# Optimization experiments

Measured on AMD Instinct MI355X. Metric: run time of the kernel, lower is better.

## Reference

```python
import jax, jax.numpy as jnp
import numpy as np

N, D, H, F, E = 2048, 1024, 16, 4096, 16
DH = D // H
CAP_F = 1.25
EPS = 1e-5

def _ln(x, w, b):
    mu = jnp.mean(x, -1, keepdims=True)
    var = jnp.mean((x - mu) ** 2, -1, keepdims=True)
    return (x - mu) * jax.lax.rsqrt(var + EPS) * w + b

def setup_inputs() -> dict:
    key = jax.random.key(0)
    ks = jax.random.split(key, 16)
    s = 0.02
    w = lambda k, shape: jax.random.normal(k, shape, jnp.float32) * s
    z = lambda *shape: jnp.zeros(shape, jnp.float32)
    return {
        'x': jax.random.normal(ks[0], (N, D), jnp.float32),
        'wk': w(ks[1], (D, D)), 'bk': z(D),
        'wq': w(ks[2], (D, D)), 'bq': z(D),
        'wv': w(ks[3], (D, D)), 'bv': z(D),
        'ipw': w(ks[4], (3 * D, D)), 'ipb': z(3 * D),
        'opw': w(ks[5], (D, D)), 'opb': z(D),
        'ln1_w': jnp.ones((D,), jnp.float32), 'ln1_b': z(D),
        'ln2_w': jnp.ones((D,), jnp.float32), 'ln2_b': z(D),
        'router_w': w(ks[6], (E, D)), 'router_b': z(E),
        'w1': w(ks[7], (E, F, D)), 'b1': z(E, F),
        'w2': w(ks[8], (E, D, F)), 'b2': z(E, D),
        'causal_mask': jnp.triu(jnp.ones((N, N), bool), k=1),  # True = masked
    }

def reference(x, wk, bk, wq, bq, wv, bv, ipw, ipb, opw, opb,
              ln1_w, ln1_b, ln2_w, ln2_b, router_w, router_b,
              w1, b1, w2, b2, causal_mask):
    n = x.shape[0]
    # --- MHA sublayer (pre-norm). NOTE: original calls multihead_attn(K, Q, V),
    # so query = W_key(h), key = W_query(h), value = W_value(h).
    h = _ln(x, ln1_w, ln1_b)
    q_in = h @ wk.T + bk
    k_in = h @ wq.T + bq
    v_in = h @ wv.T + bv
    q = (q_in @ ipw[:D].T + ipb[:D]).reshape(n, H, DH)
    k = (k_in @ ipw[D:2 * D].T + ipb[D:2 * D]).reshape(n, H, DH)
    v = (v_in @ ipw[2 * D:].T + ipb[2 * D:]).reshape(n, H, DH)
    scores = jnp.einsum('nhd,mhd->hnm', q, k) / jnp.sqrt(jnp.float32(DH))
    scores = jnp.where(causal_mask[None], -jnp.inf, scores)
    attn = jax.nn.softmax(scores, axis=-1)
    ctx = jnp.einsum('hnm,mhd->nhd', attn, v).reshape(n, D)
    x = x + ctx @ opw.T + opb
    # --- MoE FFN sublayer (pre-norm), top-1 routing with capacity drop.
    h = _ln(x, ln2_w, ln2_b)
    probs = jax.nn.softmax(h @ router_w.T + router_b, axis=-1)  # [N, E]
    p_max = jnp.max(probs, axis=-1)
    routes = jnp.argmax(probs, axis=-1)
    cap = int(CAP_F * n / E)
    onehot = jax.nn.one_hot(routes, E, dtype=jnp.int32)
    pos = jnp.cumsum(onehot, axis=0)[jnp.arange(n), routes] - 1  # position within expert
    keep = pos < cap
    slot = jnp.where(keep, routes * cap + pos, E * cap)  # dropped -> trash row
    buf = jnp.zeros((E * cap + 1, D), h.dtype).at[slot].set(h)
    xe = buf[:E * cap].reshape(E, cap, D)
    h1 = jax.nn.relu(jnp.einsum('ecd,efd->ecf', xe, w1) + b1[:, None, :])
    ye = jnp.einsum('ecf,edf->ecd', h1, w2) + b2[:, None, :]
    ybuf = jnp.concatenate([ye.reshape(E * cap, D), jnp.zeros((1, D), h.dtype)], 0)
    y = jnp.where(keep[:, None], ybuf[slot], h)  # dropped tokens pass through
    return x + y * p_max[:, None]  # is_scale_prob=True
```

## Files before the change

kernel.cpp:

```cpp
#include <hip/hip_runtime.h>
#include <hip/hip_bf16.h>


typedef unsigned int u32;
typedef unsigned short u16;
typedef __attribute__((ext_vector_type(8))) u16 u16x8;
typedef __attribute__((ext_vector_type(4))) float f32x4;
typedef __attribute__((ext_vector_type(8))) __bf16 bf16x8;

#define N_TOK 2048
#define DMODEL 1024
#define FEXP 4096
#define NEXP 16
#define CAP 160

__device__ __forceinline__ float b2f(u16 u) {
  u32 x = ((u32)u) << 16;
  return __builtin_bit_cast(float, x);
}
__device__ __forceinline__ u16 f2b(float f) {
  u32 i = __builtin_bit_cast(u32, f);
  u32 r = (i + 0x7fffu + ((i >> 16) & 1u)) >> 16;
  return (u16)r;
}

__device__ __forceinline__ f32x4 mfma16(u16x8 a, u16x8 b, f32x4 c) {
  return __builtin_amdgcn_mfma_f32_16x16x32_bf16(
      __builtin_bit_cast(bf16x8, a), __builtin_bit_cast(bf16x8, b), c, 0, 0, 0);
}

__device__ __forceinline__ void gll16(const void* g, void* lds) {
  __builtin_amdgcn_global_load_lds(
      (const __attribute__((address_space(1))) u32*)(unsigned long long)(uintptr_t)g,
      (__attribute__((address_space(3))) u32*)(u32)(uintptr_t)lds, 16, 0, 0);
}

__global__ __launch_bounds__(256) void split_kernel(const float *s, u16 *hi, u16 *lo, int n4) {
  const int i = blockIdx.x * 256 + threadIdx.x;
  if (i >= n4) return;
  const float4 v = ((const float4 *)s)[i];
  const u16 h0 = f2b(v.x), h1 = f2b(v.y), h2 = f2b(v.z), h3 = f2b(v.w);
  const u16 l0 = f2b(v.x - b2f(h0)), l1 = f2b(v.y - b2f(h1));
  const u16 l2 = f2b(v.z - b2f(h2)), l3 = f2b(v.w - b2f(h3));
  ((uint2 *)hi)[i] = make_uint2((u32)h0 | ((u32)h1 << 16), (u32)h2 | ((u32)h3 << 16));
  ((uint2 *)lo)[i] = make_uint2((u32)l0 | ((u32)l1 << 16), (u32)l2 | ((u32)l3 << 16));
}

struct GemmSP {
  const u16 *Ah, *Al; long sA; int lda;
  const u16 *Wh, *Wl; long sWp;
  const float *bias; long sB;
  const float *B0, *B1, *B2;
  const float *Rres;
  u16 *Ch, *Cl; float *Cf;
  long sC; int ldc; int K;
};

__global__ __launch_bounds__(256) void gemm_split(GemmSP p) {
  __shared__ u16 AsH[4096], AsL[4096], BsH[4096], BsL[4096];
  const int tid = threadIdx.x, lane = tid & 63, wave = tid >> 6;
  const int z = blockIdx.z;
  const int m0 = blockIdx.x * 128, n0 = blockIdx.y * 128;
  const u16 *Ah = p.Ah + (long)z * p.sA;
  const u16 *Al = p.Al + (long)z * p.sA;
  const u16 *Wh = p.Wh + (long)z * p.sWp;
  const u16 *Wl = p.Wl + (long)z * p.sWp;
  const float *bias = (p.sB >= 0) ? (p.bias + (long)z * p.sB)
                                  : (z == 0 ? p.B0 : z == 1 ? p.B1 : p.B2);
  const int K = p.K;
  const int srow = tid >> 2, scol = (tid & 3) * 8;
  const int R0 = (wave >> 1) * 64, C0 = (wave & 1) * 64;
  const int l15 = lane & 15, quad = lane >> 4;

  f32x4 acc[4][4];
#pragma unroll
  for (int i = 0; i < 4; ++i)
#pragma unroll
    for (int j = 0; j < 4; ++j) acc[i][j] = (f32x4){0.f, 0.f, 0.f, 0.f};

  for (int s = 0; s < (K >> 5); ++s) {
    const int kk = s << 5;
    __syncthreads();
#pragma unroll
    for (int h = 0; h < 2; ++h) {
      const long ao = (long)(m0 + h * 64 + srow) * p.lda + kk + scol;
      gll16(Ah + ao, &AsH[(h * 64 + wave * 16) * 32]);
      gll16(Al + ao, &AsL[(h * 64 + wave * 16) * 32]);
      const long bo = (long)(n0 + h * 64 + srow) * K + kk + scol;
      gll16(Wh + bo, &BsH[(h * 64 + wave * 16) * 32]);
      gll16(Wl + bo, &BsL[(h * 64 + wave * 16) * 32]);
    }
    __syncthreads();
    u16x8 aH[4], aL[4], bH[4], bL[4];
#pragma unroll
    for (int i = 0; i < 4; ++i) {
      aH[i] = *(const u16x8 *)&AsH[(R0 + i * 16 + l15) * 32 + quad * 8];
      aL[i] = *(const u16x8 *)&AsL[(R0 + i * 16 + l15) * 32 + quad * 8];
    }
#pragma unroll
    for (int j = 0; j < 4; ++j) {
      bH[j] = *(const u16x8 *)&BsH[(C0 + j * 16 + l15) * 32 + quad * 8];
      bL[j] = *(const u16x8 *)&BsL[(C0 + j * 16 + l15) * 32 + quad * 8];
    }
#pragma unroll
    for (int i = 0; i < 4; ++i)
#pragma unroll
      for (int j = 0; j < 4; ++j) {
        acc[i][j] = mfma16(aH[i], bH[j], acc[i][j]);
        acc[i][j] = mfma16(aL[i], bH[j], acc[i][j]);
        acc[i][j] = mfma16(aH[i], bL[j], acc[i][j]);
      }
  }

#pragma unroll
  for (int j = 0; j < 4; ++j) {
    const int n = n0 + C0 + j * 16 + l15;
    const float bv = bias[n];
#pragma unroll
    for (int i = 0; i < 4; ++i)
#pragma unroll
      for (int r = 0; r < 4; ++r) {
        const int m = m0 + R0 + i * 16 + quad * 4 + r;
        float v = acc[i][j][r] + bv;
        if (p.Rres) v += p.Rres[(long)m * p.ldc + n];
        const long idx = (long)m * p.ldc + n + (long)z * p.sC;
        if (p.Cf) p.Cf[idx] = v;
        else {
          const u16 hh = f2b(v);
          p.Ch[idx] = hh;
          p.Cl[idx] = f2b(v - b2f(hh));
        }
      }
  }
}

__device__ __forceinline__ float block_sum(float v, float *red) {
#pragma unroll
  for (int off = 32; off > 0; off >>= 1) v += __shfl_xor(v, off);
  const int w = threadIdx.x >> 6;
  __syncthreads();
  if ((threadIdx.x & 63) == 0) red[w] = v;
  __syncthreads();
  return red[0] + red[1] + red[2] + red[3];
}

__global__ __launch_bounds__(256) void ln1_kernel(const float *x, const float *w,
                                                  const float *b, u16 *Hh, u16 *Hl) {
  __shared__ float red[4];
  const int n = blockIdx.x, t = threadIdx.x;
  const float4 u = ((const float4 *)(x + (long)n * DMODEL))[t];
  float v[4] = {u.x, u.y, u.z, u.w};
  const float mean = block_sum(v[0] + v[1] + v[2] + v[3], red) * (1.f / DMODEL);
  float s2 = 0.f;
#pragma unroll
  for (int i = 0; i < 4; ++i) { float d = v[i] - mean; s2 += d * d; }
  const float var = block_sum(s2, red) * (1.f / DMODEL);
  const float rstd = 1.f / sqrtf(var + 1e-5f);
#pragma unroll
  for (int i = 0; i < 4; ++i) {
    const int c = t * 4 + i;
    const float y = (v[i] - mean) * rstd * w[c] + b[c];
    const u16 hh = f2b(y);
    Hh[(long)n * DMODEL + c] = hh;
    Hl[(long)n * DMODEL + c] = f2b(y - b2f(hh));
  }
}

__global__ __launch_bounds__(256) void ln2_kernel(const float *xin, const float *w,
                                                  const float *b, float *h2f, u16 *h2b) {
  __shared__ float red[4];
  const int n = blockIdx.x, t = threadIdx.x;
  const float4 u = ((const float4 *)(xin + (long)n * DMODEL))[t];
  float v[4] = {u.x, u.y, u.z, u.w};
  const float mean = block_sum(v[0] + v[1] + v[2] + v[3], red) * (1.f / DMODEL);
  float s2 = 0.f;
#pragma unroll
  for (int i = 0; i < 4; ++i) { float d = v[i] - mean; s2 += d * d; }
  const float var = block_sum(s2, red) * (1.f / DMODEL);
  const float rstd = 1.f / sqrtf(var + 1e-5f);
#pragma unroll
  for (int i = 0; i < 4; ++i) {
    const int c = t * 4 + i;
    const float y = (v[i] - mean) * rstd * w[c] + b[c];
    h2f[(long)n * DMODEL + c] = y;
    h2b[(long)n * DMODEL + c] = f2b(y);
  }
}

__global__ __launch_bounds__(256) void attn_kernel(const u16 *QKVh, const u16 *QKVl,
                                                   u16 *CTh, u16 *CTl) {
  __shared__ u16 Ksh[32 * 64], Ksl[32 * 64];
  __shared__ u16 Vth[64 * 33], Vtl[64 * 33];
  __shared__ u16 Psh[4 * 512], Psl[4 * 512];
  const int tid = threadIdx.x, lane = tid & 63, wave = tid >> 6;
  const int head = blockIdx.y, q0 = blockIdx.x * 64;
  const int l15 = lane & 15, quad = lane >> 4;
  const int qrow = q0 + wave * 16;

  u16x8 aQh[2], aQl[2];
  {
    const long base = (long)(qrow + l15) * 3072 + head * 64 + quad * 8;
    aQh[0] = *(const u16x8 *)(QKVh + base);
    aQh[1] = *(const u16x8 *)(QKVh + base + 32);
    aQl[0] = *(const u16x8 *)(QKVl + base);
    aQl[1] = *(const u16x8 *)(QKVl + base + 32);
  }
  f32x4 o[4];
#pragma unroll
  for (int j = 0; j < 4; ++j) o[j] = (f32x4){0.f, 0.f, 0.f, 0.f};
  f32x4 m_run = {-1e30f, -1e30f, -1e30f, -1e30f};
  f32x4 l_run = {0.f, 0.f, 0.f, 0.f};

  const int ktiles = (q0 + 64) >> 5;
  const int kr = tid >> 3, c8 = (tid & 7) * 8;

  for (int t = 0; t < ktiles; ++t) {
    const int kt0 = t << 5;
    {
      const long src = (long)(kt0 + kr) * 3072 + 1024 + head * 64 + c8;
      *(u16x8 *)&Ksh[kr * 64 + c8] = *(const u16x8 *)(QKVh + src);
      *(u16x8 *)&Ksl[kr * 64 + c8] = *(const u16x8 *)(QKVl + src);
      const u16x8 vh = *(const u16x8 *)(QKVh + src + 1024);
      const u16x8 vl = *(const u16x8 *)(QKVl + src + 1024);
#pragma unroll
      for (int jj = 0; jj < 8; ++jj) {
        Vth[(c8 + jj) * 33 + kr] = vh[jj];
        Vtl[(c8 + jj) * 33 + kr] = vl[jj];
      }
    }
    __syncthreads();
    if (kt0 <= qrow + 15) {
      f32x4 s0 = {0.f, 0.f, 0.f, 0.f}, s1 = {0.f, 0.f, 0.f, 0.f};
#pragma unroll
      for (int c = 0; c < 2; ++c) {
        const u16x8 bh0 = *(const u16x8 *)&Ksh[(l15) * 64 + c * 32 + quad * 8];
        const u16x8 bl0 = *(const u16x8 *)&Ksl[(l15) * 64 + c * 32 + quad * 8];
        const u16x8 bh1 = *(const u16x8 *)&Ksh[(16 + l15) * 64 + c * 32 + quad * 8];
        const u16x8 bl1 = *(const u16x8 *)&Ksl[(16 + l15) * 64 + c * 32 + quad * 8];
        s0 = mfma16(aQh[c], bh0, s0); s0 = mfma16(aQh[c], bl0, s0);
        s0 = mfma16(aQl[c], bh0, s0); s0 = mfma16(aQl[c], bl0, s0);
        s1 = mfma16(aQh[c], bh1, s1); s1 = mfma16(aQh[c], bl1, s1);
        s1 = mfma16(aQl[c], bh1, s1); s1 = mfma16(aQl[c], bl1, s1);
      }
      f32x4 rm;
#pragma unroll
      for (int r = 0; r < 4; ++r) {
        const int qg = qrow + quad * 4 + r;
        s0[r] *= 0.125f; s1[r] *= 0.125f;
        if (kt0 + l15 > qg) s0[r] = -1e30f;
        if (kt0 + 16 + l15 > qg) s1[r] = -1e30f;
        rm[r] = fmaxf(s0[r], s1[r]);
      }
#pragma unroll
      for (int off = 1; off < 16; off <<= 1)
#pragma unroll
        for (int r = 0; r < 4; ++r) rm[r] = fmaxf(rm[r], __shfl_xor(rm[r], off));
      f32x4 al, p0, p1, rs;
#pragma unroll
      for (int r = 0; r < 4; ++r) {
        const float mn = fmaxf(m_run[r], rm[r]);
        al[r] = expf(m_run[r] - mn);
        p0[r] = expf(s0[r] - mn);
        p1[r] = expf(s1[r] - mn);
        m_run[r] = mn;
        rs[r] = p0[r] + p1[r];
      }
#pragma unroll
      for (int off = 1; off < 16; off <<= 1)
#pragma unroll
        for (int r = 0; r < 4; ++r) rs[r] += __shfl_xor(rs[r], off);
#pragma unroll
      for (int r = 0; r < 4; ++r) l_run[r] = l_run[r] * al[r] + rs[r];
#pragma unroll
      for (int j4 = 0; j4 < 4; ++j4)
#pragma unroll
        for (int r = 0; r < 4; ++r) o[j4][r] *= al[r];
#pragma unroll
      for (int r = 0; r < 4; ++r) {
        const int rl = quad * 4 + r;
        const u16 h0 = f2b(p0[r]);
        Psh[wave * 512 + rl * 32 + l15] = h0;
        Psl[wave * 512 + rl * 32 + l15] = f2b(p0[r] - b2f(h0));
        const u16 h1 = f2b(p1[r]);
        Psh[wave * 512 + rl * 32 + 16 + l15] = h1;
        Psl[wave * 512 + rl * 32 + 16 + l15] = f2b(p1[r] - b2f(h1));
      }
      const u16x8 aPh = *(const u16x8 *)&Psh[wave * 512 + l15 * 32 + quad * 8];
      const u16x8 aPl = *(const u16x8 *)&Psl[wave * 512 + l15 * 32 + quad * 8];
#pragma unroll
      for (int j4 = 0; j4 < 4; ++j4) {
        u16x8 bvh, bvl;
#pragma unroll
        for (int jj = 0; jj < 8; ++jj) {
          bvh[jj] = Vth[(j4 * 16 + l15) * 33 + quad * 8 + jj];
          bvl[jj] = Vtl[(j4 * 16 + l15) * 33 + quad * 8 + jj];
        }
        o[j4] = mfma16(aPh, bvh, o[j4]);
        o[j4] = mfma16(aPh, bvl, o[j4]);
        o[j4] = mfma16(aPl, bvh, o[j4]);
      }
    }
    __syncthreads();
  }
#pragma unroll
  for (int j4 = 0; j4 < 4; ++j4)
#pragma unroll
    for (int r = 0; r < 4; ++r) {
      const float v = o[j4][r] / l_run[r];
      const long row = qrow + quad * 4 + r;
      const long col = head * 64 + j4 * 16 + l15;
      const u16 hh = f2b(v);
      CTh[row * 1024 + col] = hh;
      CTl[row * 1024 + col] = f2b(v - b2f(hh));
    }
}

__global__ __launch_bounds__(64) void router_kernel(const float *h2f, const float *rw,
                                                    const float *rb, float *pmax, int *route) {
  const int n = blockIdx.x, lane = threadIdx.x;
  const int e = lane >> 2, j = lane & 3;
  const float4 *wp = (const float4 *)(rw + (long)e * DMODEL + j * 256);
  const float4 *hp = (const float4 *)(h2f + (long)n * DMODEL + j * 256);
  float acc = 0.f;
  for (int i = 0; i < 64; ++i) {
    const float4 w = wp[i], h = hp[i];
    acc += h.x * w.x + h.y * w.y + h.z * w.z + h.w * w.w;
  }
  acc += __shfl_xor(acc, 1);
  acc += __shfl_xor(acc, 2);
  float lv[16];
#pragma unroll
  for (int ee = 0; ee < 16; ++ee) lv[ee] = __shfl(acc, ee * 4) + rb[ee];
  float mx = lv[0]; int am = 0;
#pragma unroll
  for (int ee = 1; ee < 16; ++ee)
    if (lv[ee] > mx) { mx = lv[ee]; am = ee; }
  float sum = 0.f;
#pragma unroll
  for (int ee = 0; ee < 16; ++ee) sum += expf(lv[ee] - mx);
  if (lane == 0) { pmax[n] = 1.f / sum; route[n] = am; }
}

__global__ __launch_bounds__(64) void scan_kernel(const int *route, int *slot, int cap) {
  const int e = blockIdx.x, lane = threadIdx.x;
  int base = 0;
  for (int i = 0; i < N_TOK / 64; ++i) {
    const int n = i * 64 + lane;
    const bool m = (route[n] == e);
    const unsigned long long bal = __ballot(m);
    if (m) {
      const int pos = base + __popcll(bal & ((1ull << lane) - 1ull));
      slot[n] = (pos < cap) ? e * cap + pos : -1;
    }
    base += __popcll(bal);
  }
}

__global__ __launch_bounds__(256) void gather_kernel(const u16 *h2b, const int *slot, u16 *xe) {
  const int n = blockIdx.x;
  const int s = slot[n];
  if (s < 0) return;
  ((uint2 *)(xe + (long)s * DMODEL))[threadIdx.x] =
      ((const uint2 *)(h2b + (long)n * DMODEL))[threadIdx.x];
}

struct MoeP {
  const u16 *A; long sA; int lda;
  const float *W; long sW;
  const float *bias; long sB;
  u16 *C; long sC; int ldc;
  int M, K, relu;
};

__global__ __launch_bounds__(256) void gemm_moe(MoeP p) {
  __shared__ u16 As[256 * 32];
  __shared__ float Bs[64 * 36];
  const int tid = threadIdx.x, lane = tid & 63, wave = tid >> 6;
  const int z = blockIdx.z, n0 = blockIdx.y * 64;
  const u16 *A = p.A + (long)z * p.sA;
  const float *W = p.W + (long)z * p.sW;
  const float *bias = p.bias + (long)z * p.sB;
  const int srow = tid >> 2, scol = (tid & 3) * 8;
  const int R0 = wave * 64;
  const int l15 = lane & 15, quad = lane >> 4;

  f32x4 acc[4][4];
#pragma unroll
  for (int i = 0; i < 4; ++i)
#pragma unroll
    for (int j = 0; j < 4; ++j) acc[i][j] = (f32x4){0.f, 0.f, 0.f, 0.f};

  for (int s = 0; s < (p.K >> 5); ++s) {
    const int kk = s << 5;
    __syncthreads();
#pragma unroll
    for (int h = 0; h < 4; ++h) {
      int ar = h * 64 + srow;
      if (ar >= p.M) ar = p.M - 1;
      gll16(A + (long)ar * p.lda + kk + scol, &As[(h * 64 + wave * 16) * 32]);
    }
    {
      const int br = tid >> 2, bc = (tid & 3) * 8;
      const float4 *src = (const float4 *)(W + (long)(n0 + br) * p.K + kk + bc);
      const float4 f0 = src[0], f1 = src[1];
      *(float4 *)&Bs[br * 36 + bc] = f0;
      *(float4 *)&Bs[br * 36 + bc + 4] = f1;
    }
    __syncthreads();
    u16x8 a[4], b[4];
#pragma unroll
    for (int i = 0; i < 4; ++i)
      a[i] = *(const u16x8 *)&As[(R0 + i * 16 + l15) * 32 + quad * 8];
#pragma unroll
    for (int j = 0; j < 4; ++j) {
      const float4 f0 = *(const float4 *)&Bs[(j * 16 + l15) * 36 + quad * 8];
      const float4 f1 = *(const float4 *)&Bs[(j * 16 + l15) * 36 + quad * 8 + 4];
      b[j][0] = f2b(f0.x); b[j][1] = f2b(f0.y); b[j][2] = f2b(f0.z); b[j][3] = f2b(f0.w);
      b[j][4] = f2b(f1.x); b[j][5] = f2b(f1.y); b[j][6] = f2b(f1.z); b[j][7] = f2b(f1.w);
    }
#pragma unroll
    for (int i = 0; i < 4; ++i)
#pragma unroll
      for (int j = 0; j < 4; ++j) acc[i][j] = mfma16(a[i], b[j], acc[i][j]);
  }

#pragma unroll
  for (int j = 0; j < 4; ++j) {
    const int n = n0 + j * 16 + l15;
    const float bv = bias[n];
#pragma unroll
    for (int i = 0; i < 4; ++i)
#pragma unroll
      for (int r = 0; r < 4; ++r) {
        const int m = R0 + i * 16 + quad * 4 + r;
        if (m >= p.M) continue;
        float v = acc[i][j][r] + bv;
        if (p.relu) v = v > 0.f ? v : 0.f;
        p.C[(long)m * p.ldc + n + (long)z * p.sC] = f2b(v);
      }
  }
}

__global__ __launch_bounds__(256) void combine_kernel(const float *x2, const float *h2f,
                                                      const u16 *ye, const float *pmax,
                                                      const int *slot, float *out) {
  const int n = blockIdx.x, t = threadIdx.x;
  const float pm = pmax[n];
  const int s = slot[n];
  float y[4];
  if (s >= 0) {
    const uint2 u = ((const uint2 *)(ye + (long)s * DMODEL))[t];
    y[0] = b2f((u16)(u.x & 0xffff)); y[1] = b2f((u16)(u.x >> 16));
    y[2] = b2f((u16)(u.y & 0xffff)); y[3] = b2f((u16)(u.y >> 16));
  } else {
    const float4 hv = ((const float4 *)(h2f + (long)n * DMODEL))[t];
    y[0] = hv.x; y[1] = hv.y; y[2] = hv.z; y[3] = hv.w;
  }
  const float4 xv = ((const float4 *)(x2 + (long)n * DMODEL))[t];
  float4 ov;
  ov.x = xv.x + pm * y[0]; ov.y = xv.y + pm * y[1];
  ov.z = xv.z + pm * y[2]; ov.w = xv.w + pm * y[3];
  ((float4 *)(out + (long)n * DMODEL))[t] = ov;
}

extern "C" void kernel_launch(void* const* d_in, const int* in_sizes, int n_in,
                              void* d_out, int out_size, void* d_ws, size_t ws_size,
                              hipStream_t stream) {
  const float *x    = (const float *)d_in[0];
  const float *wk   = (const float *)d_in[1],  *bk  = (const float *)d_in[2];
  const float *wq   = (const float *)d_in[3],  *bq  = (const float *)d_in[4];
  const float *wv   = (const float *)d_in[5],  *bv  = (const float *)d_in[6];
  const float *ipw  = (const float *)d_in[7],  *ipb = (const float *)d_in[8];
  const float *opw  = (const float *)d_in[9],  *opb = (const float *)d_in[10];
  const float *ln1w = (const float *)d_in[11], *ln1b = (const float *)d_in[12];
  const float *ln2w = (const float *)d_in[13], *ln2b = (const float *)d_in[14];
  const float *rw   = (const float *)d_in[15], *rb  = (const float *)d_in[16];
  const float *w1   = (const float *)d_in[17], *b1  = (const float *)d_in[18];
  const float *w2   = (const float *)d_in[19], *b2  = (const float *)d_in[20];

  char *ws = (char *)d_ws;
  const size_t MB = 1ull << 20;
  u16 *WqkvH = (u16 *)(ws + 0 * MB);
  u16 *WqkvL = (u16 *)(ws + 6 * MB);
  u16 *IpH   = (u16 *)(ws + 12 * MB);
  u16 *IpL   = (u16 *)(ws + 18 * MB);
  u16 *OpH   = (u16 *)(ws + 24 * MB);
  u16 *OpL   = (u16 *)(ws + 26 * MB);
  u16 *Hh    = (u16 *)(ws + 28 * MB);
  u16 *Hl    = (u16 *)(ws + 32 * MB);
  u16 *G1h   = (u16 *)(ws + 36 * MB);
  u16 *G1l   = (u16 *)(ws + 48 * MB);
  u16 *Qh    = (u16 *)(ws + 0 * MB);
  u16 *Ql    = (u16 *)(ws + 60 * MB);
  u16 *CTh   = (u16 *)(ws + 28 * MB);
  u16 *CTl   = (u16 *)(ws + 32 * MB);
  float *x2  = (float *)(ws + 56 * MB);
  float *h2f = (float *)(ws + 64 * MB);
  u16 *h2b   = (u16 *)(ws + 72 * MB);
  float *pmax = (float *)(ws + 76 * MB);
  int *route  = (int *)(ws + 76 * MB + 32768);
  int *slot   = (int *)(ws + 76 * MB + 65536);
  u16 *xe  = (u16 *)(ws + 20 * MB);
  u16 *h1e = (u16 *)(ws + 0 * MB);
  u16 *ye  = (u16 *)(ws + 26 * MB);

  split_kernel<<<1024, 256, 0, stream>>>(wk, WqkvH, WqkvL, 1024 * 1024 / 4);
  split_kernel<<<1024, 256, 0, stream>>>(wq, WqkvH + 1024 * 1024, WqkvL + 1024 * 1024, 1024 * 1024 / 4);
  split_kernel<<<1024, 256, 0, stream>>>(wv, WqkvH + 2 * 1024 * 1024, WqkvL + 2 * 1024 * 1024, 1024 * 1024 / 4);
  split_kernel<<<3072, 256, 0, stream>>>(ipw, IpH, IpL, 3 * 1024 * 1024 / 4);
  split_kernel<<<1024, 256, 0, stream>>>(opw, OpH, OpL, 1024 * 1024 / 4);

  ln1_kernel<<<N_TOK, 256, 0, stream>>>(x, ln1w, ln1b, Hh, Hl);

  {
    GemmSP p{};
    p.Ah = Hh; p.Al = Hl; p.sA = 0; p.lda = 1024;
    p.Wh = WqkvH; p.Wl = WqkvL; p.sWp = 1024 * 1024;
    p.sB = -1; p.B0 = bk; p.B1 = bq; p.B2 = bv;
    p.Ch = G1h; p.Cl = G1l; p.sC = 1024; p.ldc = 3072; p.K = 1024;
    gemm_split<<<dim3(16, 8, 3), 256, 0, stream>>>(p);
  }
  {
    GemmSP p{};
    p.Ah = G1h; p.Al = G1l; p.sA = 1024; p.lda = 3072;
    p.Wh = IpH; p.Wl = IpL; p.sWp = 1024 * 1024;
    p.bias = ipb; p.sB = 1024;
    p.Ch = Qh; p.Cl = Ql; p.sC = 1024; p.ldc = 3072; p.K = 1024;
    gemm_split<<<dim3(16, 8, 3), 256, 0, stream>>>(p);
  }
  attn_kernel<<<dim3(32, 16), 256, 0, stream>>>(Qh, Ql, CTh, CTl);

  {
    GemmSP p{};
    p.Ah = CTh; p.Al = CTl; p.sA = 0; p.lda = 1024;
    p.Wh = OpH; p.Wl = OpL; p.sWp = 0;
    p.bias = opb; p.sB = 0;
    p.Rres = x;
    p.Cf = x2; p.sC = 0; p.ldc = 1024; p.K = 1024;
    gemm_split<<<dim3(16, 8, 1), 256, 0, stream>>>(p);
  }
  ln2_kernel<<<N_TOK, 256, 0, stream>>>(x2, ln2w, ln2b, h2f, h2b);
  router_kernel<<<N_TOK, 64, 0, stream>>>(h2f, rw, rb, pmax, route);
  scan_kernel<<<NEXP, 64, 0, stream>>>(route, slot, CAP);
  gather_kernel<<<N_TOK, 256, 0, stream>>>(h2b, slot, xe);
  {
    MoeP p{};
    p.A = xe; p.sA = (long)CAP * 1024; p.lda = 1024;
    p.W = w1; p.sW = (long)FEXP * 1024;
    p.bias = b1; p.sB = FEXP;
    p.C = h1e; p.sC = (long)CAP * FEXP; p.ldc = FEXP;
    p.M = CAP; p.K = 1024; p.relu = 1;
    gemm_moe<<<dim3(1, 64, NEXP), 256, 0, stream>>>(p);
  }
  {
    MoeP p{};
    p.A = h1e; p.sA = (long)CAP * FEXP; p.lda = FEXP;
    p.W = w2; p.sW = (long)1024 * FEXP;
    p.bias = b2; p.sB = 1024;
    p.C = ye; p.sC = (long)CAP * 1024; p.ldc = 1024;
    p.M = CAP; p.K = FEXP; p.relu = 0;
    gemm_moe<<<dim3(1, 16, NEXP), 256, 0, stream>>>(p);
  }
  combine_kernel<<<N_TOK, 256, 0, stream>>>(x2, h2f, ye, pmax, slot, (float *)d_out);
}
```

Measured before the change: 1.252 ms.

## Pipeline attention K/V loads, pre-transpose V, balance causal tiles, split MoE GEMM rows

Adds a separate kernel that transposes V into a global [head*64, N] layout so attention loads V tiles with vector loads instead of scalar transposed stores. Attention now double-buffers K/V in shared memory with register prefetch, remaps blocks so heavy and light causal query tiles are paired, drops one low-order MFMA term in the QK product, and uses exp2 with a folded scale. The MoE GEMM converts weights to bf16 once when staging and splits the 160-row M dimension across two blocks to raise parallelism. Dropping the Ql*Kl term slightly reduces QK precision, and the extra transpose kernel adds a launch and memory traffic.

```diff
diff --git a/kernel.cpp b/kernel.cpp
--- a/kernel.cpp
+++ b/kernel.cpp
@@ -187,13 +187,48 @@
   }
 }
 
+__global__ __launch_bounds__(256) void vtrans_kernel(const u16 *QKVh, const u16 *QKVl,
+                                                     u16 *Vtgh, u16 *Vtgl) {
+  __shared__ u16 Th[64][72], Tl[64][72];
+  const int n0 = blockIdx.x * 64, c0 = blockIdx.y * 64;
+  const int t = threadIdx.x;
+  const int r = t >> 2, cc = (t & 3) * 16;
+  {
+    const long src = (long)(n0 + r) * 3072 + 2048 + c0 + cc;
+    *(u16x8 *)&Th[r][cc] = *(const u16x8 *)(QKVh + src);
+    *(u16x8 *)&Th[r][cc + 8] = *(const u16x8 *)(QKVh + src + 8);
+    *(u16x8 *)&Tl[r][cc] = *(const u16x8 *)(QKVl + src);
+    *(u16x8 *)&Tl[r][cc + 8] = *(const u16x8 *)(QKVl + src + 8);
+  }
+  __syncthreads();
+  u16x8 oh[2], ol[2];
+#pragma unroll
+  for (int j = 0; j < 2; ++j)
+#pragma unroll
+    for (int k = 0; k < 8; ++k) {
+      oh[j][k] = Th[cc + j * 8 + k][r];
+      ol[j][k] = Tl[cc + j * 8 + k][r];
+    }
+  const long dst = (long)(c0 + r) * 2048 + n0 + cc;
+  *(u16x8 *)(Vtgh + dst) = oh[0];
+  *(u16x8 *)(Vtgh + dst + 8) = oh[1];
+  *(u16x8 *)(Vtgl + dst) = ol[0];
+  *(u16x8 *)(Vtgl + dst + 8) = ol[1];
+}
+
 __global__ __launch_bounds__(256) void attn_kernel(const u16 *QKVh, const u16 *QKVl,
+                                                   const u16 *Vtgh, const u16 *Vtgl,
                                                    u16 *CTh, u16 *CTl) {
-  __shared__ u16 Ksh[32 * 64], Ksl[32 * 64];
-  __shared__ u16 Vth[64 * 33], Vtl[64 * 33];
-  __shared__ u16 Psh[4 * 512], Psl[4 * 512];
+  __shared__ u16 Ksh[2][32][72], Ksl[2][32][72];
+  __shared__ u16 Vsh[2][64][40], Vsl[2][64][40];
+  __shared__ u16 Psh[4][16][40], Psl[4][16][40];
   const int tid = threadIdx.x, lane = tid & 63, wave = tid >> 6;
-  const int head = blockIdx.y, q0 = blockIdx.x * 64;
+  const int id = blockIdx.x;
+  const int uu = id & 255, hi = id >> 8, pp = uu & 1, up = uu >> 1;
+  const int g = up >> 2;
+  const int qb = (pp ^ hi) ? (31 - g) : g;
+  const int head = ((up & 3) << 2) | (pp << 1) | hi;
+  const int q0 = qb * 64;
   const int l15 = lane & 15, quad = lane >> 4;
   const int qrow = q0 + wave * 16;
 
@@ -212,41 +247,58 @@
   f32x4 l_run = {0.f, 0.f, 0.f, 0.f};
 
   const int ktiles = (q0 + 64) >> 5;
-  const int kr = tid >> 3, c8 = (tid & 7) * 8;
+  const int kr = tid >> 3, kc = (tid & 7) * 8;
+  const int vr = tid >> 2, vc = (tid & 3) * 8;
+  const long kgbase = 1024 + head * 64 + kc;
+  const long vgbase = (long)(head * 64 + vr) * 2048 + vc;
+
+  u16x8 skh, skl, svh, svl;
+  {
+    const long ks = (long)kr * 3072 + kgbase;
+    skh = *(const u16x8 *)(QKVh + ks);
+    skl = *(const u16x8 *)(QKVl + ks);
+    svh = *(const u16x8 *)(Vtgh + vgbase);
+    svl = *(const u16x8 *)(Vtgl + vgbase);
+    *(u16x8 *)&Ksh[0][kr][kc] = skh;
+    *(u16x8 *)&Ksl[0][kr][kc] = skl;
+    *(u16x8 *)&Vsh[0][vr][vc] = svh;
+    *(u16x8 *)&Vsl[0][vr][vc] = svl;
+  }
+  __syncthreads();
+
+  constexpr float SC = 0.125f * 1.4426950408889634f;
 
   for (int t = 0; t < ktiles; ++t) {
+    const int b = t & 1;
     const int kt0 = t << 5;
-    {
-      const long src = (long)(kt0 + kr) * 3072 + 1024 + head * 64 + c8;
-      *(u16x8 *)&Ksh[kr * 64 + c8] = *(const u16x8 *)(QKVh + src);
-      *(u16x8 *)&Ksl[kr * 64 + c8] = *(const u16x8 *)(QKVl + src);
-      const u16x8 vh = *(const u16x8 *)(QKVh + src + 1024);
-      const u16x8 vl = *(const u16x8 *)(QKVl + src + 1024);
-#pragma unroll
-      for (int jj = 0; jj < 8; ++jj) {
-        Vth[(c8 + jj) * 33 + kr] = vh[jj];
-        Vtl[(c8 + jj) * 33 + kr] = vl[jj];
-      }
-    }
-    __syncthreads();
+    const bool pf = (t + 1 < ktiles);
+    if (pf) {
+      const long ks = (long)(kt0 + 32 + kr) * 3072 + kgbase;
+      skh = *(const u16x8 *)(QKVh + ks);
+      skl = *(const u16x8 *)(QKVl + ks);
+      svh = *(const u16x8 *)(Vtgh + vgbase + kt0 + 32);
+      svl = *(const u16x8 *)(Vtgl + vgbase + kt0 + 32);
+    }
     if (kt0 <= qrow + 15) {
       f32x4 s0 = {0.f, 0.f, 0.f, 0.f}, s1 = {0.f, 0.f, 0.f, 0.f};
 #pragma unroll
       for (int c = 0; c < 2; ++c) {
-        const u16x8 bh0 = *(const u16x8 *)&Ksh[(l15) * 64 + c * 32 + quad * 8];
-        const u16x8 bl0 = *(const u16x8 *)&Ksl[(l15) * 64 + c * 32 + quad * 8];
-        const u16x8 bh1 = *(const u16x8 *)&Ksh[(16 + l15) * 64 + c * 32 + quad * 8];
-        const u16x8 bl1 = *(const u16x8 *)&Ksl[(16 + l15) * 64 + c * 32 + quad * 8];
-        s0 = mfma16(aQh[c], bh0, s0); s0 = mfma16(aQh[c], bl0, s0);
-        s0 = mfma16(aQl[c], bh0, s0); s0 = mfma16(aQl[c], bl0, s0);
-        s1 = mfma16(aQh[c], bh1, s1); s1 = mfma16(aQh[c], bl1, s1);
-        s1 = mfma16(aQl[c], bh1, s1); s1 = mfma16(aQl[c], bl1, s1);
+        const u16x8 bh0 = *(const u16x8 *)&Ksh[b][l15][c * 32 + quad * 8];
+        const u16x8 bl0 = *(const u16x8 *)&Ksl[b][l15][c * 32 + quad * 8];
+        const u16x8 bh1 = *(const u16x8 *)&Ksh[b][16 + l15][c * 32 + quad * 8];
+        const u16x8 bl1 = *(const u16x8 *)&Ksl[b][16 + l15][c * 32 + quad * 8];
+        s0 = mfma16(aQh[c], bh0, s0);
+        s0 = mfma16(aQl[c], bh0, s0);
+        s0 = mfma16(aQh[c], bl0, s0);
+        s1 = mfma16(aQh[c], bh1, s1);
+        s1 = mfma16(aQl[c], bh1, s1);
+        s1 = mfma16(aQh[c], bl1, s1);
       }
       f32x4 rm;
 #pragma unroll
       for (int r = 0; r < 4; ++r) {
         const int qg = qrow + quad * 4 + r;
-        s0[r] *= 0.125f; s1[r] *= 0.125f;
+        s0[r] *= SC; s1[r] *= SC;
         if (kt0 + l15 > qg) s0[r] = -1e30f;
         if (kt0 + 16 + l15 > qg) s1[r] = -1e30f;
         rm[r] = fmaxf(s0[r], s1[r]);
@@ -259,9 +311,9 @@
 #pragma unroll
       for (int r = 0; r < 4; ++r) {
         const float mn = fmaxf(m_run[r], rm[r]);
-        al[r] = expf(m_run[r] - mn);
-        p0[r] = expf(s0[r] - mn);
-        p1[r] = expf(s1[r] - mn);
+        al[r] = exp2f(m_run[r] - mn);
+        p0[r] = exp2f(s0[r] - mn);
+        p1[r] = exp2f(s1[r] - mn);
         m_run[r] = mn;
         rs[r] = p0[r] + p1[r];
       }
@@ -279,26 +331,29 @@
       for (int r = 0; r < 4; ++r) {
         const int rl = quad * 4 + r;
         const u16 h0 = f2b(p0[r]);
-        Psh[wave * 512 + rl * 32 + l15] = h0;
-        Psl[wave * 512 + rl * 32 + l15] = f2b(p0[r] - b2f(h0));
+        Psh[wave][rl][l15] = h0;
+        Psl[wave][rl][l15] = f2b(p0[r] - b2f(h0));
         const u16 h1 = f2b(p1[r]);
-        Psh[wave * 512 + rl * 32 + 16 + l15] = h1;
-        Psl[wave * 512 + rl * 32 + 16 + l15] = f2b(p1[r] - b2f(h1));
-      }
-      const u16x8 aPh = *(const u16x8 *)&Psh[wave * 512 + l15 * 32 + quad * 8];
-      const u16x8 aPl = *(const u16x8 *)&Psl[wave * 512 + l15 * 32 + quad * 8];
+        Psh[wave][rl][16 + l15] = h1;
+        Psl[wave][rl][16 + l15] = f2b(p1[r] - b2f(h1));
+      }
+      const u16x8 aPh = *(const u16x8 *)&Psh[wave][l15][quad * 8];
+      const u16x8 aPl = *(const u16x8 *)&Psl[wave][l15][quad * 8];
 #pragma unroll
       for (int j4 = 0; j4 < 4; ++j4) {
-        u16x8 bvh, bvl;
-#pragma unroll
-        for (int jj = 0; jj < 8; ++jj) {
-          bvh[jj] = Vth[(j4 * 16 + l15) * 33 + quad * 8 + jj];
-          bvl[jj] = Vtl[(j4 * 16 + l15) * 33 + quad * 8 + jj];
-        }
+        const u16x8 bvh = *(const u16x8 *)&Vsh[b][j4 * 16 + l15][quad * 8];
+        const u16x8 bvl = *(const u16x8 *)&Vsl[b][j4 * 16 + l15][quad * 8];
         o[j4] = mfma16(aPh, bvh, o[j4]);
         o[j4] = mfma16(aPh, bvl, o[j4]);
         o[j4] = mfma16(aPl, bvh, o[j4]);
       }
+    }
+    if (pf) {
+      const int b2 = b ^ 1;
+      *(u16x8 *)&Ksh[b2][kr][kc] = skh;
+      *(u16x8 *)&Ksl[b2][kr][kc] = skl;
+      *(u16x8 *)&Vsh[b2][vr][vc] = svh;
+      *(u16x8 *)&Vsl[b2][vr][vc] = svl;
     }
     __syncthreads();
   }
@@ -373,20 +428,20 @@
 };
 
 __global__ __launch_bounds__(256) void gemm_moe(MoeP p) {
-  __shared__ u16 As[256 * 32];
-  __shared__ float Bs[64 * 36];
+  __shared__ u16 As[128 * 32];
+  __shared__ u16 Bs[64][40];
   const int tid = threadIdx.x, lane = tid & 63, wave = tid >> 6;
-  const int z = blockIdx.z, n0 = blockIdx.y * 64;
+  const int z = blockIdx.z, n0 = blockIdx.y * 64, m0 = blockIdx.x * 128;
   const u16 *A = p.A + (long)z * p.sA;
   const float *W = p.W + (long)z * p.sW;
   const float *bias = p.bias + (long)z * p.sB;
   const int srow = tid >> 2, scol = (tid & 3) * 8;
-  const int R0 = wave * 64;
+  const int R0 = wave * 32;
   const int l15 = lane & 15, quad = lane >> 4;
 
-  f32x4 acc[4][4];
-#pragma unroll
-  for (int i = 0; i < 4; ++i)
+  f32x4 acc[2][4];
+#pragma unroll
+  for (int i = 0; i < 2; ++i)
 #pragma unroll
     for (int j = 0; j < 4; ++j) acc[i][j] = (f32x4){0.f, 0.f, 0.f, 0.f};
 
@@ -394,8 +449,8 @@
     const int kk = s << 5;
     __syncthreads();
 #pragma unroll
-    for (int h = 0; h < 4; ++h) {
-      int ar = h * 64 + srow;
+    for (int h = 0; h < 2; ++h) {
+      int ar = m0 + h * 64 + srow;
       if (ar >= p.M) ar = p.M - 1;
       gll16(A + (long)ar * p.lda + kk + scol, &As[(h * 64 + wave * 16) * 32]);
     }
@@ -403,23 +458,21 @@
       const int br = tid >> 2, bc = (tid & 3) * 8;
       const float4 *src = (const float4 *)(W + (long)(n0 + br) * p.K + kk + bc);
       const float4 f0 = src[0], f1 = src[1];
-      *(float4 *)&Bs[br * 36 + bc] = f0;
-      *(float4 *)&Bs[br * 36 + bc + 4] = f1;
+      u16x8 bv;
+      bv[0] = f2b(f0.x); bv[1] = f2b(f0.y); bv[2] = f2b(f0.z); bv[3] = f2b(f0.w);
+      bv[4] = f2b(f1.x); bv[5] = f2b(f1.y); bv[6] = f2b(f1.z); bv[7] = f2b(f1.w);
+      *(u16x8 *)&Bs[br][bc] = bv;
     }
     __syncthreads();
-    u16x8 a[4], b[4];
-#pragma unroll
-    for (int i = 0; i < 4; ++i)
+    u16x8 a[2], b[4];
+#pragma unroll
+    for (int i = 0; i < 2; ++i)
       a[i] = *(const u16x8 *)&As[(R0 + i * 16 + l15) * 32 + quad * 8];
 #pragma unroll
-    for (int j = 0; j < 4; ++j) {
-      const float4 f0 = *(const float4 *)&Bs[(j * 16 + l15) * 36 + quad * 8];
-      const float4 f1 = *(const float4 *)&Bs[(j * 16 + l15) * 36 + quad * 8 + 4];
-      b[j][0] = f2b(f0.x); b[j][1] = f2b(f0.y); b[j][2] = f2b(f0.z); b[j][3] = f2b(f0.w);
-      b[j][4] = f2b(f1.x); b[j][5] = f2b(f1.y); b[j][6] = f2b(f1.z); b[j][7] = f2b(f1.w);
-    }
-#pragma unroll
-    for (int i = 0; i < 4; ++i)
+    for (int j = 0; j < 4; ++j)
+      b[j] = *(const u16x8 *)&Bs[j * 16 + l15][quad * 8];
+#pragma unroll
+    for (int i = 0; i < 2; ++i)
 #pragma unroll
       for (int j = 0; j < 4; ++j) acc[i][j] = mfma16(a[i], b[j], acc[i][j]);
   }
@@ -429,10 +482,10 @@
     const int n = n0 + j * 16 + l15;
     const float bv = bias[n];
 #pragma unroll
-    for (int i = 0; i < 4; ++i)
+    for (int i = 0; i < 2; ++i)
 #pragma unroll
       for (int r = 0; r < 4; ++r) {
-        const int m = R0 + i * 16 + quad * 4 + r;
+        const int m = m0 + R0 + i * 16 + quad * 4 + r;
         if (m >= p.M) continue;
         float v = acc[i][j][r] + bv;
         if (p.relu) v = v > 0.f ? v : 0.f;
@@ -492,6 +545,8 @@
   u16 *G1l   = (u16 *)(ws + 48 * MB);
   u16 *Qh    = (u16 *)(ws + 0 * MB);
   u16 *Ql    = (u16 *)(ws + 60 * MB);
+  u16 *Vtgh  = (u16 *)(ws + 36 * MB);
+  u16 *Vtgl  = (u16 *)(ws + 40 * MB);
   u16 *CTh   = (u16 *)(ws + 28 * MB);
   u16 *CTl   = (u16 *)(ws + 32 * MB);
   float *x2  = (float *)(ws + 56 * MB);
@@ -528,7 +583,9 @@
     p.Ch = Qh; p.Cl = Ql; p.sC = 1024; p.ldc = 3072; p.K = 1024;
     gemm_split<<<dim3(16, 8, 3), 256, 0, stream>>>(p);
   }
-  attn_kernel<<<dim3(32, 16), 256, 0, stream>>>(Qh, Ql, CTh, CTl);
+  vtrans_kernel<<<dim3(32, 16), 256, 0, stream>>>(Qh, Ql, Vtgh, Vtgl);
+
+  attn_kernel<<<dim3(512), 256, 0, stream>>>(Qh, Ql, Vtgh, Vtgl, CTh, CTl);
 
   {
     GemmSP p{};
@@ -550,7 +607,7 @@
     p.bias = b1; p.sB = FEXP;
     p.C = h1e; p.sC = (long)CAP * FEXP; p.ldc = FEXP;
     p.M = CAP; p.K = 1024; p.relu = 1;
-    gemm_moe<<<dim3(1, 64, NEXP), 256, 0, stream>>>(p);
+    gemm_moe<<<dim3(2, 64, NEXP), 256, 0, stream>>>(p);
   }
   {
     MoeP p{};
@@ -559,7 +616,7 @@
     p.bias = b2; p.sB = 1024;
     p.C = ye; p.sC = (long)CAP * 1024; p.ldc = 1024;
     p.M = CAP; p.K = FEXP; p.relu = 0;
-    gemm_moe<<<dim3(1, 16, NEXP), 256, 0, stream>>>(p);
+    gemm_moe<<<dim3(2, 16, NEXP), 256, 0, stream>>>(p);
   }
   combine_kernel<<<N_TOK, 256, 0, stream>>>(x2, h2f, ye, pmax, slot, (float *)d_out);
 }
```

Result: faster. 1.052 ms (-15.9%).
